# Performance work log

Measured on AMD Instinct MI355X. Metric: run time of the kernel, lower is better.

## Reference

```python
import jax, jax.numpy as jnp
import numpy as np

WS = 7
NH = 4

def _rel_idx(ws):
    ch, cw = np.meshgrid(np.arange(ws), np.arange(ws), indexing='ij')
    cf = np.stack([ch.ravel(), cw.ravel()])  # [2, ws*ws]
    rel = cf[:, :, None] - cf[:, None, :]
    rel = rel.transpose(1, 2, 0)
    rel[:, :, 0] += ws - 1
    rel[:, :, 1] += ws - 1
    rel[:, :, 0] *= 2 * ws - 1
    return jnp.asarray(rel.sum(-1), dtype=jnp.int32)  # [N, N]

def layernorm(x, g, b, eps=1e-5):
    m = jnp.mean(x, -1, keepdims=True)
    v = jnp.var(x, -1, keepdims=True)
    return (x - m) * jax.lax.rsqrt(v + eps) * g + b

def setup_inputs() -> dict:
    key = jax.random.key(0)
    ks = jax.random.split(key, 8)
    B, HH, WW, C = 32, 56, 56, 128
    hid = 512
    s = 0.02
    return {
        'x': jax.random.normal(ks[0], (B, HH * WW, C), jnp.float32),
        'H': HH, 'W': WW,
        'norm1_g': jnp.ones((C,), jnp.float32),
        'norm1_b': jnp.zeros((C,), jnp.float32),
        'qkv_w': jax.random.normal(ks[1], (3 * C, C), jnp.float32) * s,
        'qkv_b': jnp.zeros((3 * C,), jnp.float32),
        'rel_bias_table': jax.random.normal(ks[2], ((2 * WS - 1) ** 2, NH), jnp.float32) * s,
        'rel_idx': _rel_idx(WS),
        'proj_w': jax.random.normal(ks[3], (C, C), jnp.float32) * s,
        'proj_b': jnp.zeros((C,), jnp.float32),
        'norm2_g': jnp.ones((C,), jnp.float32),
        'norm2_b': jnp.zeros((C,), jnp.float32),
        'mlp_w1': jax.random.normal(ks[4], (hid, C), jnp.float32) * s,
        'mlp_b1': jnp.zeros((hid,), jnp.float32),
        'mlp_w2': jax.random.normal(ks[5], (C, hid), jnp.float32) * s,
        'mlp_b2': jnp.zeros((C,), jnp.float32),
    }

def swin_block(x, H, W, norm1_g, norm1_b, qkv_w, qkv_b, rel_bias_table, rel_idx,
               proj_w, proj_b, norm2_g, norm2_b, mlp_w1, mlp_b1, mlp_w2, mlp_b2,
               shift=3, ws=WS, nh=NH):
    B, L, C = x.shape
    N = ws * ws
    hd = C // nh
    scale = hd ** -0.5
    shortcut = x
    h = layernorm(x, norm1_g, norm1_b).reshape(B, H, W, C)
    if shift > 0:
        h = jnp.roll(h, (-shift, -shift), axis=(1, 2))
    # window partition -> [B*nW, N, C]
    h = h.reshape(B, H // ws, ws, W // ws, ws, C).transpose(0, 1, 3, 2, 4, 5).reshape(-1, N, C)
    # attention (no mask in source forward)
    qkv = h @ qkv_w.T + qkv_b  # [B_, N, 3C]
    qkv = qkv.reshape(-1, N, 3, nh, hd).transpose(2, 0, 3, 1, 4)
    q, k, v = qkv[0] * scale, qkv[1], qkv[2]  # [B_, nh, N, hd]
    attn = jnp.einsum('bhnd,bhmd->bhnm', q, k)
    bias = rel_bias_table[rel_idx.reshape(-1)].reshape(N, N, nh).transpose(2, 0, 1)
    attn = jax.nn.softmax(attn + bias[None], axis=-1)
    o = jnp.einsum('bhnm,bhmd->bhnd', attn, v).transpose(0, 2, 1, 3).reshape(-1, N, C)
    o = o @ proj_w.T + proj_b
    # window reverse -> [B, H, W, C]
    o = o.reshape(B, H // ws, W // ws, ws, ws, C).transpose(0, 1, 3, 2, 4, 5).reshape(B, H, W, C)
    if shift > 0:
        o = jnp.roll(o, (shift, shift), axis=(1, 2))
    x = shortcut + o.reshape(B, L, C)
    h2 = layernorm(x, norm2_g, norm2_b)
    h2 = jax.nn.gelu(h2 @ mlp_w1.T + mlp_b1, approximate=False) @ mlp_w2.T + mlp_b2
    return x + h2

def reference(x, H, W, norm1_g, norm1_b, qkv_w, qkv_b, rel_bias_table, rel_idx,
              proj_w, proj_b, norm2_g, norm2_b, mlp_w1, mlp_b1, mlp_w2, mlp_b2):
    return swin_block(x, H, W, norm1_g, norm1_b, qkv_w, qkv_b, rel_bias_table, rel_idx,
                      proj_w, proj_b, norm2_g, norm2_b, mlp_w1, mlp_b1, mlp_w2, mlp_b2)
```

## Files before the change

kernel.cpp:

```cpp
#include <hip/hip_runtime.h>
#include <hip/hip_bf16.h>


#define NWIN 2048

typedef short short8  __attribute__((ext_vector_type(8)));
typedef short short4v __attribute__((ext_vector_type(4)));
typedef float f32x4   __attribute__((ext_vector_type(4)));

#define QKVW_OFF  0
#define PROJW_OFF 49152
#define W1_OFF    65536
#define W2_OFF    131072
#define BIAS_BYTE_OFF 393216

__device__ __forceinline__ short f2bs(float v) {
  __hip_bfloat16 h = __float2bfloat16(v);
  union { __hip_bfloat16 h; short s; } u; u.h = h; return u.s;
}
__device__ __forceinline__ float gelu_f(float v) {
  float u = v * (0.7978845608028654f + 0.03567740814f * v * v);
  return v * __builtin_amdgcn_rcpf(1.f + __expf(-2.f * u));
}

__global__ __launch_bounds__(256) void conv_kernel(
    const float* __restrict__ qkvw, const float* __restrict__ projw,
    const float* __restrict__ w1,   const float* __restrict__ w2,
    const float* __restrict__ tab,  const int* __restrict__ ridx,
    __hip_bfloat16* __restrict__ wsb, float* __restrict__ biasT)
{
  int idx = blockIdx.x * 256 + threadIdx.x;
  if (idx < 49152)       wsb[QKVW_OFF + idx]          = __float2bfloat16(qkvw[idx]);
  else if (idx < 65536)  wsb[PROJW_OFF + idx - 49152] = __float2bfloat16(projw[idx - 49152]);
  else if (idx < 131072) wsb[W1_OFF + idx - 65536]    = __float2bfloat16(w1[idx - 65536]);
  else if (idx < 196608) wsb[W2_OFF + idx - 131072]   = __float2bfloat16(w2[idx - 131072]);
  else if (idx < 212992) {
    int i = idx - 196608;
    int h = i >> 12, m = (i >> 6) & 63, n = i & 63;
    biasT[i] = (m < 49 && n < 49) ? tab[ridx[n*49 + m]*4 + h] : 0.f;
  }
}

__global__ __launch_bounds__(512, 4) void fused_kernel(
    const float* __restrict__ x,
    const float* __restrict__ n1g, const float* __restrict__ n1b,
    const __hip_bfloat16* __restrict__ qkvwb, const float* __restrict__ qkvb,
    const float* __restrict__ biasT,
    const __hip_bfloat16* __restrict__ projwb, const float* __restrict__ projb,
    const float* __restrict__ n2g, const float* __restrict__ n2b,
    const __hip_bfloat16* __restrict__ w1b, const float* __restrict__ b1,
    const __hip_bfloat16* __restrict__ w2b, const float* __restrict__ b2,
    float* __restrict__ out)
{
  __shared__ alignas(16) __hip_bfloat16 hbuf[64][136];
  __shared__ alignas(16) char regA[40960];
  __shared__ alignas(16) __hip_bfloat16 vT[4][32][72];
  __hip_bfloat16* const qkb = (__hip_bfloat16*)regA;
  float*          const x2s = (float*)regA;
  __hip_bfloat16* const hb  = (__hip_bfloat16*)regA;

  const int tid = threadIdx.x, wave = tid >> 6, lane = tid & 63;
  const int l15 = lane & 15, quad = lane >> 4;
  const int b = blockIdx.x >> 6, wi = (blockIdx.x >> 3) & 7, wj = blockIdx.x & 7;

  {
    float g0 = n1g[lane], g1 = n1g[lane+64], e0 = n1b[lane], e1 = n1b[lane+64];
    float va[7], vb[7];
    #pragma unroll
    for (int i = 0; i < 7; ++i) {
      int n = wave + i*8;
      va[i] = 0.f; vb[i] = 0.f;
      if (n < 49) {
        int r = n / 7, c = n - r * 7;
        int si = wi*7 + r + 3; if (si >= 56) si -= 56;
        int sj = wj*7 + c + 3; if (sj >= 56) sj -= 56;
        const float* xr = x + (b*3136 + si*56 + sj) * 128;
        va[i] = xr[lane]; vb[i] = xr[lane + 64];
      }
    }
    #pragma unroll
    for (int i = 0; i < 7; ++i) {
      int n = wave + i*8;
      if (n < 49) {
        float s = va[i] + vb[i], sq = va[i]*va[i] + vb[i]*vb[i];
        #pragma unroll
        for (int off = 32; off > 0; off >>= 1) {
          s  += __shfl_xor(s,  off);
          sq += __shfl_xor(sq, off);
        }
        float mean = s * 0.0078125f;
        float var  = sq * 0.0078125f - mean*mean;
        float rstd = rsqrtf(var + 1e-5f);
        hbuf[n][lane]    = __float2bfloat16((va[i]-mean)*rstd*g0 + e0);
        hbuf[n][lane+64] = __float2bfloat16((vb[i]-mean)*rstd*g1 + e1);
      }
    }
  }
  __syncthreads();

  {
    const int t0 = wave * 3;
    f32x4 acc[3][4] = {};
    #pragma unroll
    for (int ks = 0; ks < 4; ++ks) {
      short8 hf[4];
      #pragma unroll
      for (int mt = 0; mt < 4; ++mt)
        hf[mt] = *(const short8*)(&hbuf[mt*16 + l15][ks*32 + quad*8]);
      #pragma unroll
      for (int ft = 0; ft < 3; ++ft) {
        short8 wf = *(const short8*)(qkvwb + ((t0 + ft)*16 + l15)*128 + ks*32 + quad*8);
        #pragma unroll
        for (int mt = 0; mt < 4; ++mt)
          acc[ft][mt] = __builtin_amdgcn_mfma_f32_16x16x32_bf16(wf, hf[mt], acc[ft][mt], 0, 0, 0);
      }
    }
    #pragma unroll
    for (int ft = 0; ft < 3; ++ft) {
      const int t = t0 + ft;
      if (t < 16) {
        const int which = t >> 3;
        const int fo = (t & 7) * 16 + quad * 4;
        const int hh = fo >> 5, d0 = fo & 31;
        const float qs = (t < 8) ? 0.17677669529663687f : 1.0f;
        float bb[4];
        #pragma unroll
        for (int r = 0; r < 4; ++r) bb[r] = qkvb[which*128 + fo + r];
        #pragma unroll
        for (int mt = 0; mt < 4; ++mt) {
          int m = mt*16 + l15;
          if (m < 49) {
            short4v pk;
            #pragma unroll
            for (int r = 0; r < 4; ++r) pk[r] = f2bs((acc[ft][mt][r] + bb[r]) * qs);
            *(short4v*)(qkb + ((hh*2 + which)*64 + m)*40 + d0) = pk;
          }
        }
      } else {
        const int nf = (t - 16) * 16 + quad * 4;
        const int hh = nf >> 5, d0 = nf & 31;
        float bb[4];
        #pragma unroll
        for (int r = 0; r < 4; ++r) bb[r] = qkvb[256 + nf + r];
        #pragma unroll
        for (int mt = 0; mt < 4; ++mt) {
          int m = mt*16 + l15;
          #pragma unroll
          for (int r = 0; r < 4; ++r) {
            float v = (m < 49) ? (acc[ft][mt][r] + bb[r]) : 0.f;
            vT[hh][d0 + r][m] = __float2bfloat16(v);
          }
        }
      }
    }
  }
  __syncthreads();

  {
    const int h = wave >> 1, half = wave & 1;
    __hip_bfloat16* qbase = qkb + (h*2 + 0)*64*40;
    __hip_bfloat16* kbase = qkb + (h*2 + 1)*64*40;
    short8 kf[4], qf[2];
    #pragma unroll
    for (int mt = 0; mt < 4; ++mt) kf[mt] = *(const short8*)(kbase + (mt*16 + l15)*40 + quad*8);
    #pragma unroll
    for (int nt = 0; nt < 2; ++nt)
      qf[nt] = *(const short8*)(qbase + ((half*2 + nt)*16 + l15)*40 + quad*8);
    const float* bT = biasT + h*4096;
    float bv[4][2][4];
    #pragma unroll
    for (int mt = 0; mt < 4; ++mt)
      #pragma unroll
      for (int nt = 0; nt < 2; ++nt)
        #pragma unroll
        for (int r = 0; r < 4; ++r)
          bv[mt][nt][r] = bT[(mt*16 + quad*4 + r)*64 + (half*2 + nt)*16 + l15];
    __syncthreads();

    f32x4 sacc[4][2] = {};
    #pragma unroll
    for (int mt = 0; mt < 4; ++mt)
      #pragma unroll
      for (int nt = 0; nt < 2; ++nt)
        sacc[mt][nt] = __builtin_amdgcn_mfma_f32_16x16x32_bf16(kf[mt], qf[nt], sacc[mt][nt], 0, 0, 0);

    #pragma unroll
    for (int mt = 0; mt < 4; ++mt)
      #pragma unroll
      for (int nt = 0; nt < 2; ++nt)
        #pragma unroll
        for (int r = 0; r < 4; ++r)
          sacc[mt][nt][r] += bv[mt][nt][r];

    __hip_bfloat16* pb = qbase;
    #pragma unroll
    for (int nt = 0; nt < 2; ++nt) {
      float mx = -1e30f;
      #pragma unroll
      for (int mt = 0; mt < 3; ++mt)
        #pragma unroll
        for (int r = 0; r < 4; ++r) mx = fmaxf(mx, sacc[mt][nt][r]);
      mx = fmaxf(mx, (quad == 0) ? sacc[3][nt][0] : -1e30f);
      mx = fmaxf(mx, __shfl_xor(mx, 16));
      mx = fmaxf(mx, __shfl_xor(mx, 32));
      float sum = 0.f;
      #pragma unroll
      for (int mt = 0; mt < 3; ++mt)
        #pragma unroll
        for (int r = 0; r < 4; ++r) {
          float e = __expf(sacc[mt][nt][r] - mx);
          sacc[mt][nt][r] = e; sum += e;
        }
      {
        float e = (quad == 0) ? __expf(sacc[3][nt][0] - mx) : 0.f;
        sacc[3][nt][0] = e; sacc[3][nt][1] = 0.f; sacc[3][nt][2] = 0.f; sacc[3][nt][3] = 0.f;
        sum += e;
      }
      sum += __shfl_xor(sum, 16);
      sum += __shfl_xor(sum, 32);
      float inv = 1.f / sum;
      int n = (half*2 + nt)*16 + l15;
      #pragma unroll
      for (int mt = 0; mt < 4; ++mt) {
        short4v pk;
        #pragma unroll
        for (int r = 0; r < 4; ++r) pk[r] = f2bs(sacc[mt][nt][r] * inv);
        *(short4v*)(pb + n*72 + mt*16 + quad*4) = pk;
      }
    }

    f32x4 oacc[2][2] = {};
    #pragma unroll
    for (int kt = 0; kt < 2; ++kt) {
      short8 vf[2], pf[2];
      #pragma unroll
      for (int dt = 0; dt < 2; ++dt)
        vf[dt] = *(const short8*)(&vT[h][dt*16 + l15][kt*32 + quad*8]);
      #pragma unroll
      for (int nc = 0; nc < 2; ++nc)
        pf[nc] = *(const short8*)(pb + ((half*2 + nc)*16 + l15)*72 + kt*32 + quad*8);
      #pragma unroll
      for (int dt = 0; dt < 2; ++dt)
        #pragma unroll
        for (int nc = 0; nc < 2; ++nc)
          oacc[dt][nc] = __builtin_amdgcn_mfma_f32_16x16x32_bf16(vf[dt], pf[nc], oacc[dt][nc], 0, 0, 0);
    }
    #pragma unroll
    for (int dt = 0; dt < 2; ++dt)
      #pragma unroll
      for (int nc = 0; nc < 2; ++nc) {
        int n = (half*2 + nc)*16 + l15;
        if (n < 49) {
          short4v pk;
          #pragma unroll
          for (int r = 0; r < 4; ++r) pk[r] = f2bs(oacc[dt][nc][r]);
          *(short4v*)(&hbuf[n][h*32 + dt*16 + quad*4]) = pk;
        }
      }
  }
  __syncthreads();

  f32x4 x2v[4];
  {
    const int ncol0 = wave * 16;
    const int n = ncol0 + l15;
    float xres[4][4];
    #pragma unroll
    for (int mt = 0; mt < 4; ++mt) {
      #pragma unroll
      for (int r = 0; r < 4; ++r) {
        int m = mt*16 + quad*4 + r;
        float v = 0.f;
        if (m < 49) {
          int rr = m / 7, cc = m - rr * 7;
          int si = wi*7 + rr + 3; if (si >= 56) si -= 56;
          int sj = wj*7 + cc + 3; if (sj >= 56) sj -= 56;
          v = x[(b*3136 + si*56 + sj) * 128 + n];
        }
        xres[mt][r] = v;
      }
    }
    f32x4 acc[4] = {};
    #pragma unroll
    for (int ks = 0; ks < 4; ++ks) {
      short8 af[4];
      #pragma unroll
      for (int mt = 0; mt < 4; ++mt)
        af[mt] = *(const short8*)(&hbuf[mt*16 + l15][ks*32 + quad*8]);
      short8 bfr = *(const short8*)(projwb + (ncol0 + l15)*128 + ks*32 + quad*8);
      #pragma unroll
      for (int mt = 0; mt < 4; ++mt)
        acc[mt] = __builtin_amdgcn_mfma_f32_16x16x32_bf16(af[mt], bfr, acc[mt], 0, 0, 0);
    }
    float pbv = projb[n];
    #pragma unroll
    for (int mt = 0; mt < 4; ++mt) {
      #pragma unroll
      for (int r = 0; r < 4; ++r) {
        int m = mt*16 + quad*4 + r;
        float v = 0.f;
        if (m < 49) v = acc[mt][r] + pbv + xres[mt][r];
        x2v[mt][r] = v;
        x2s[m*132 + n] = v;
      }
    }
  }
  __syncthreads();

  {
    float g0 = n2g[lane], g1 = n2g[lane+64], e0 = n2b[lane], e1 = n2b[lane+64];
    for (int n = wave; n < 49; n += 8) {
      float v0 = x2s[n*132 + lane], v1 = x2s[n*132 + lane + 64];
      float s = v0 + v1, sq = v0*v0 + v1*v1;
      #pragma unroll
      for (int off = 32; off > 0; off >>= 1) {
        s  += __shfl_xor(s,  off);
        sq += __shfl_xor(sq, off);
      }
      float mean = s * 0.0078125f;
      float var  = sq * 0.0078125f - mean*mean;
      float rstd = rsqrtf(var + 1e-5f);
      hbuf[n][lane]    = __float2bfloat16((v0-mean)*rstd*g0 + e0);
      hbuf[n][lane+64] = __float2bfloat16((v1-mean)*rstd*g1 + e1);
    }
    __hip_bfloat16 z = __float2bfloat16(0.f);
    for (int n = 49 + wave; n < 64; n += 8) {
      hbuf[n][lane] = z; hbuf[n][lane+64] = z;
    }
  }
  __syncthreads();

  f32x4 acc2[4] = {};
  #pragma unroll
  for (int chunk = 0; chunk < 2; ++chunk) {
    {
      const int jbl = wave * 32;
      f32x4 acc1[2][4] = {};
      #pragma unroll
      for (int ks = 0; ks < 4; ++ks) {
        short8 lf[4];
        #pragma unroll
        for (int mt = 0; mt < 4; ++mt)
          lf[mt] = *(const short8*)(&hbuf[mt*16 + l15][ks*32 + quad*8]);
        #pragma unroll
        for (int jt = 0; jt < 2; ++jt) {
          short8 wf = *(const short8*)(w1b + (chunk*256 + jbl + jt*16 + l15)*128 + ks*32 + quad*8);
          #pragma unroll
          for (int mt = 0; mt < 4; ++mt)
            acc1[jt][mt] = __builtin_amdgcn_mfma_f32_16x16x32_bf16(wf, lf[mt], acc1[jt][mt], 0, 0, 0);
        }
      }
      #pragma unroll
      for (int jt = 0; jt < 2; ++jt) {
        int j0l = jbl + jt*16 + quad*4;
        float bb[4];
        #pragma unroll
        for (int r = 0; r < 4; ++r) bb[r] = b1[chunk*256 + j0l + r];
        #pragma unroll
        for (int mt = 0; mt < 4; ++mt) {
          int m = mt*16 + l15;
          short4v pk;
          #pragma unroll
          for (int r = 0; r < 4; ++r) pk[r] = f2bs(gelu_f(acc1[jt][mt][r] + bb[r]));
          *(short4v*)(hb + m*264 + j0l) = pk;
        }
      }
    }
    __syncthreads();

    {
      const int fb2 = wave * 16;
      #pragma unroll
      for (int ks = 0; ks < 8; ++ks) {
        short8 af[4];
        #pragma unroll
        for (int mt = 0; mt < 4; ++mt)
          af[mt] = *(const short8*)(hb + (mt*16 + l15)*264 + ks*32 + quad*8);
        short8 bfr = *(const short8*)(w2b + (fb2 + l15)*512 + chunk*256 + ks*32 + quad*8);
        #pragma unroll
        for (int mt = 0; mt < 4; ++mt)
          acc2[mt] = __builtin_amdgcn_mfma_f32_16x16x32_bf16(af[mt], bfr, acc2[mt], 0, 0, 0);
      }
    }
    if (chunk == 0) __syncthreads();
  }

  {
    const int f = wave * 16 + l15;
    const float bb = b2[f];
    #pragma unroll
    for (int mt = 0; mt < 4; ++mt) {
      #pragma unroll
      for (int r = 0; r < 4; ++r) {
        int m = mt*16 + quad*4 + r;
        if (m < 49) {
          int rr = m / 7, cc = m - rr * 7;
          int si = wi*7 + rr + 3; if (si >= 56) si -= 56;
          int sj = wj*7 + cc + 3; if (sj >= 56) sj -= 56;
          int o = (b*3136 + si*56 + sj) * 128 + f;
          out[o] = acc2[mt][r] + bb + x2v[mt][r];
        }
      }
    }
  }
}

extern "C" void kernel_launch(void* const* d_in, const int* in_sizes, int n_in,
                              void* d_out, int out_size, void* d_ws, size_t ws_size,
                              hipStream_t stream) {
  const float* x     = (const float*)d_in[0];
  const float* n1g   = (const float*)d_in[3];
  const float* n1b   = (const float*)d_in[4];
  const float* qkvw  = (const float*)d_in[5];
  const float* qkvb  = (const float*)d_in[6];
  const float* tab   = (const float*)d_in[7];
  const int*   ridx  = (const int*)d_in[8];
  const float* projw = (const float*)d_in[9];
  const float* projb = (const float*)d_in[10];
  const float* n2g   = (const float*)d_in[11];
  const float* n2b   = (const float*)d_in[12];
  const float* w1    = (const float*)d_in[13];
  const float* b1    = (const float*)d_in[14];
  const float* w2    = (const float*)d_in[15];
  const float* b2    = (const float*)d_in[16];
  float* outp = (float*)d_out;

  __hip_bfloat16* wsb = (__hip_bfloat16*)d_ws;
  float* biasT = (float*)((char*)d_ws + BIAS_BYTE_OFF);

  hipLaunchKernelGGL(conv_kernel, dim3(832), dim3(256), 0, stream,
                     qkvw, projw, w1, w2, tab, ridx, wsb, biasT);
  hipLaunchKernelGGL(fused_kernel, dim3(NWIN), dim3(512), 0, stream,
                     x, n1g, n1b, wsb + QKVW_OFF, qkvb, biasT, wsb + PROJW_OFF, projb,
                     n2g, n2b, wsb + W1_OFF, b1, wsb + W2_OFF, b2, outp);
}
```

Before: 262.1 us.

## Prefetch weight fragments into registers ahead of barriers across GEMM stages

The fused Swin block kernel now issues global loads of weight fragments into registers earlier: QKV weights at kernel start, the proj weights and residual x during the attention stage, and W1 chunk 0 and W2 fragments before the preceding barriers. The MLP chunk loop is manually unrolled so that each W2 slice is loaded before its sync. The aim is to hide global and L2 load latency behind LDS work and barriers instead of stalling in front of the MFMAs. In exchange, register pressure rises considerably (dozens of extra short8 values live at once), which could lower occupancy or cause spills.

```diff
diff --git a/kernel.cpp b/kernel.cpp
--- a/kernel.cpp
+++ b/kernel.cpp
@@ -63,6 +63,16 @@
   const int l15 = lane & 15, quad = lane >> 4;
   const int b = blockIdx.x >> 6, wi = (blockIdx.x >> 3) & 7, wj = blockIdx.x & 7;
 
+  short8 wreg[3][4];
+  {
+    const int t0 = wave * 3;
+    #pragma unroll
+    for (int ft = 0; ft < 3; ++ft)
+      #pragma unroll
+      for (int ks = 0; ks < 4; ++ks)
+        wreg[ft][ks] = *(const short8*)(qkvwb + ((t0 + ft)*16 + l15)*128 + ks*32 + quad*8);
+  }
+
   {
     float g0 = n1g[lane], g1 = n1g[lane+64], e0 = n1b[lane], e1 = n1b[lane+64];
     float va[7], vb[7];
@@ -109,10 +119,9 @@
         hf[mt] = *(const short8*)(&hbuf[mt*16 + l15][ks*32 + quad*8]);
       #pragma unroll
       for (int ft = 0; ft < 3; ++ft) {
-        short8 wf = *(const short8*)(qkvwb + ((t0 + ft)*16 + l15)*128 + ks*32 + quad*8);
         #pragma unroll
         for (int mt = 0; mt < 4; ++mt)
-          acc[ft][mt] = __builtin_amdgcn_mfma_f32_16x16x32_bf16(wf, hf[mt], acc[ft][mt], 0, 0, 0);
+          acc[ft][mt] = __builtin_amdgcn_mfma_f32_16x16x32_bf16(wreg[ft][ks], hf[mt], acc[ft][mt], 0, 0, 0);
       }
     }
     #pragma unroll
@@ -156,6 +165,8 @@
   }
   __syncthreads();
 
+  short8 pw[4];
+  float xres[4][4];
   {
     const int h = wave >> 1, half = wave & 1;
     __hip_bfloat16* qbase = qkb + (h*2 + 0)*64*40;
@@ -257,14 +268,11 @@
           *(short4v*)(&hbuf[n][h*32 + dt*16 + quad*4]) = pk;
         }
       }
-  }
-  __syncthreads();
-
-  f32x4 x2v[4];
-  {
-    const int ncol0 = wave * 16;
-    const int n = ncol0 + l15;
-    float xres[4][4];
+
+    const int ncol0 = wave * 16, n4 = ncol0 + l15;
+    #pragma unroll
+    for (int ks = 0; ks < 4; ++ks)
+      pw[ks] = *(const short8*)(projwb + n4*128 + ks*32 + quad*8);
     #pragma unroll
     for (int mt = 0; mt < 4; ++mt) {
       #pragma unroll
@@ -275,11 +283,17 @@
           int rr = m / 7, cc = m - rr * 7;
           int si = wi*7 + rr + 3; if (si >= 56) si -= 56;
           int sj = wj*7 + cc + 3; if (sj >= 56) sj -= 56;
-          v = x[(b*3136 + si*56 + sj) * 128 + n];
+          v = x[(b*3136 + si*56 + sj) * 128 + n4];
         }
         xres[mt][r] = v;
       }
     }
+  }
+  __syncthreads();
+
+  f32x4 x2v[4];
+  {
+    const int n = wave * 16 + l15;
     f32x4 acc[4] = {};
     #pragma unroll
     for (int ks = 0; ks < 4; ++ks) {
@@ -287,10 +301,9 @@
       #pragma unroll
       for (int mt = 0; mt < 4; ++mt)
         af[mt] = *(const short8*)(&hbuf[mt*16 + l15][ks*32 + quad*8]);
-      short8 bfr = *(const short8*)(projwb + (ncol0 + l15)*128 + ks*32 + quad*8);
       #pragma unroll
       for (int mt = 0; mt < 4; ++mt)
-        acc[mt] = __builtin_amdgcn_mfma_f32_16x16x32_bf16(af[mt], bfr, acc[mt], 0, 0, 0);
+        acc[mt] = __builtin_amdgcn_mfma_f32_16x16x32_bf16(af[mt], pw[ks], acc[mt], 0, 0, 0);
     }
     float pbv = projb[n];
     #pragma unroll
@@ -328,65 +341,121 @@
       hbuf[n][lane] = z; hbuf[n][lane+64] = z;
     }
   }
+
+  short8 w1f0[4][2];
+  {
+    const int jbl = wave * 32;
+    #pragma unroll
+    for (int ks = 0; ks < 4; ++ks)
+      #pragma unroll
+      for (int jt = 0; jt < 2; ++jt)
+        w1f0[ks][jt] = *(const short8*)(w1b + (jbl + jt*16 + l15)*128 + ks*32 + quad*8);
+  }
   __syncthreads();
 
   f32x4 acc2[4] = {};
+  short8 w2f[8];
+  const int fb2 = wave * 16;
+
+  {
+    const int jbl = wave * 32;
+    f32x4 acc1[2][4] = {};
+    #pragma unroll
+    for (int ks = 0; ks < 4; ++ks) {
+      short8 lf[4];
+      #pragma unroll
+      for (int mt = 0; mt < 4; ++mt)
+        lf[mt] = *(const short8*)(&hbuf[mt*16 + l15][ks*32 + quad*8]);
+      #pragma unroll
+      for (int jt = 0; jt < 2; ++jt)
+        #pragma unroll
+        for (int mt = 0; mt < 4; ++mt)
+          acc1[jt][mt] = __builtin_amdgcn_mfma_f32_16x16x32_bf16(w1f0[ks][jt], lf[mt], acc1[jt][mt], 0, 0, 0);
+    }
+    #pragma unroll
+    for (int jt = 0; jt < 2; ++jt) {
+      int j0l = jbl + jt*16 + quad*4;
+      float bb[4];
+      #pragma unroll
+      for (int r = 0; r < 4; ++r) bb[r] = b1[j0l + r];
+      #pragma unroll
+      for (int mt = 0; mt < 4; ++mt) {
+        int m = mt*16 + l15;
+        short4v pk;
+        #pragma unroll
+        for (int r = 0; r < 4; ++r) pk[r] = f2bs(gelu_f(acc1[jt][mt][r] + bb[r]));
+        *(short4v*)(hb + m*264 + j0l) = pk;
+      }
+    }
+  }
   #pragma unroll
-  for (int chunk = 0; chunk < 2; ++chunk) {
-    {
-      const int jbl = wave * 32;
-      f32x4 acc1[2][4] = {};
-      #pragma unroll
-      for (int ks = 0; ks < 4; ++ks) {
-        short8 lf[4];
+  for (int ks = 0; ks < 8; ++ks)
+    w2f[ks] = *(const short8*)(w2b + (fb2 + l15)*512 + ks*32 + quad*8);
+  __syncthreads();
+
+  #pragma unroll
+  for (int ks = 0; ks < 8; ++ks) {
+    short8 af[4];
+    #pragma unroll
+    for (int mt = 0; mt < 4; ++mt)
+      af[mt] = *(const short8*)(hb + (mt*16 + l15)*264 + ks*32 + quad*8);
+    #pragma unroll
+    for (int mt = 0; mt < 4; ++mt)
+      acc2[mt] = __builtin_amdgcn_mfma_f32_16x16x32_bf16(af[mt], w2f[ks], acc2[mt], 0, 0, 0);
+  }
+  __syncthreads();
+
+  {
+    const int jbl = wave * 32;
+    f32x4 acc1[2][4] = {};
+    #pragma unroll
+    for (int ks = 0; ks < 4; ++ks) {
+      short8 lf[4];
+      #pragma unroll
+      for (int mt = 0; mt < 4; ++mt)
+        lf[mt] = *(const short8*)(&hbuf[mt*16 + l15][ks*32 + quad*8]);
+      #pragma unroll
+      for (int jt = 0; jt < 2; ++jt) {
+        short8 wf = *(const short8*)(w1b + (256 + jbl + jt*16 + l15)*128 + ks*32 + quad*8);
         #pragma unroll
         for (int mt = 0; mt < 4; ++mt)
-          lf[mt] = *(const short8*)(&hbuf[mt*16 + l15][ks*32 + quad*8]);
-        #pragma unroll
-        for (int jt = 0; jt < 2; ++jt) {
-          short8 wf = *(const short8*)(w1b + (chunk*256 + jbl + jt*16 + l15)*128 + ks*32 + quad*8);
-          #pragma unroll
-          for (int mt = 0; mt < 4; ++mt)
-            acc1[jt][mt] = __builtin_amdgcn_mfma_f32_16x16x32_bf16(wf, lf[mt], acc1[jt][mt], 0, 0, 0);
-        }
-      }
-      #pragma unroll
-      for (int jt = 0; jt < 2; ++jt) {
-        int j0l = jbl + jt*16 + quad*4;
-        float bb[4];
-        #pragma unroll
-        for (int r = 0; r < 4; ++r) bb[r] = b1[chunk*256 + j0l + r];
-        #pragma unroll
-        for (int mt = 0; mt < 4; ++mt) {
-          int m = mt*16 + l15;
-          short4v pk;
-          #pragma unroll
-          for (int r = 0; r < 4; ++r) pk[r] = f2bs(gelu_f(acc1[jt][mt][r] + bb[r]));
-          *(short4v*)(hb + m*264 + j0l) = pk;
-        }
-      }
-    }
-    __syncthreads();
-
-    {
-      const int fb2 = wave * 16;
-      #pragma unroll
-      for (int ks = 0; ks < 8; ++ks) {
-        short8 af[4];
-        #pragma unroll
-        for (int mt = 0; mt < 4; ++mt)
-          af[mt] = *(const short8*)(hb + (mt*16 + l15)*264 + ks*32 + quad*8);
-        short8 bfr = *(const short8*)(w2b + (fb2 + l15)*512 + chunk*256 + ks*32 + quad*8);
-        #pragma unroll
-        for (int mt = 0; mt < 4; ++mt)
-          acc2[mt] = __builtin_amdgcn_mfma_f32_16x16x32_bf16(af[mt], bfr, acc2[mt], 0, 0, 0);
-      }
-    }
-    if (chunk == 0) __syncthreads();
-  }
-
-  {
-    const int f = wave * 16 + l15;
+          acc1[jt][mt] = __builtin_amdgcn_mfma_f32_16x16x32_bf16(wf, lf[mt], acc1[jt][mt], 0, 0, 0);
+      }
+    }
+    #pragma unroll
+    for (int jt = 0; jt < 2; ++jt) {
+      int j0l = jbl + jt*16 + quad*4;
+      float bb[4];
+      #pragma unroll
+      for (int r = 0; r < 4; ++r) bb[r] = b1[256 + j0l + r];
+      #pragma unroll
+      for (int mt = 0; mt < 4; ++mt) {
+        int m = mt*16 + l15;
+        short4v pk;
+        #pragma unroll
+        for (int r = 0; r < 4; ++r) pk[r] = f2bs(gelu_f(acc1[jt][mt][r] + bb[r]));
+        *(short4v*)(hb + m*264 + j0l) = pk;
+      }
+    }
+  }
+  #pragma unroll
+  for (int ks = 0; ks < 8; ++ks)
+    w2f[ks] = *(const short8*)(w2b + (fb2 + l15)*512 + 256 + ks*32 + quad*8);
+  __syncthreads();
+
+  #pragma unroll
+  for (int ks = 0; ks < 8; ++ks) {
+    short8 af[4];
+    #pragma unroll
+    for (int mt = 0; mt < 4; ++mt)
+      af[mt] = *(const short8*)(hb + (mt*16 + l15)*264 + ks*32 + quad*8);
+    #pragma unroll
+    for (int mt = 0; mt < 4; ++mt)
+      acc2[mt] = __builtin_amdgcn_mfma_f32_16x16x32_bf16(af[mt], w2f[ks], acc2[mt], 0, 0, 0);
+  }
+
+  {
+    const int f = fb2 + l15;
     const float bb = b2[f];
     #pragma unroll
     for (int mt = 0; mt < 4; ++mt) {
```

New measurement: 256.7 us, median of 2. 1.02x faster.

## Cut LDS footprint: keep Q/P in registers, swizzle V, double-buffer MLP chunks

Applied to the files above, without the earlier changes.

Q is now computed per wave directly in registers and the softmax probabilities are repacked into MFMA fragments with lane shuffles, so neither round-trips through shared memory. V is stored transposed with an XOR swizzle to avoid bank conflicts. The MLP hidden layer is split into four 128-wide chunks over two ping-pong LDS buffers, which lets GEMM1 of one chunk overlap GEMM2 of the previous one. Total LDS shrinks and launch bounds rise from 4 to 6 blocks per CU to raise occupancy, at the risk of register pressure and extra shuffle work.

```diff
diff --git a/kernel.cpp b/kernel.cpp
--- a/kernel.cpp
+++ b/kernel.cpp
@@ -7,6 +7,8 @@
 typedef short short8  __attribute__((ext_vector_type(8)));
 typedef short short4v __attribute__((ext_vector_type(4)));
 typedef float f32x4   __attribute__((ext_vector_type(4)));
+
+union Frag { int i[4]; unsigned u[4]; short8 s; };
 
 #define QKVW_OFF  0
 #define PROJW_OFF 49152
@@ -41,7 +43,7 @@
   }
 }
 
-__global__ __launch_bounds__(512, 4) void fused_kernel(
+__global__ __launch_bounds__(512, 6) void fused_kernel(
     const float* __restrict__ x,
     const float* __restrict__ n1g, const float* __restrict__ n1b,
     const __hip_bfloat16* __restrict__ qkvwb, const float* __restrict__ qkvb,
@@ -53,14 +55,16 @@
     float* __restrict__ out)
 {
   __shared__ alignas(16) __hip_bfloat16 hbuf[64][136];
-  __shared__ alignas(16) char regA[40960];
-  __shared__ alignas(16) __hip_bfloat16 vT[4][32][72];
-  __hip_bfloat16* const qkb = (__hip_bfloat16*)regA;
-  float*          const x2s = (float*)regA;
-  __hip_bfloat16* const hb  = (__hip_bfloat16*)regA;
+  __shared__ alignas(16) char shmem[36864];
+  __hip_bfloat16* const Kl  = (__hip_bfloat16*)shmem;
+  __hip_bfloat16* const vTl = (__hip_bfloat16*)(shmem + 20480);
+  float*          const x2s = (float*)shmem;
+  __hip_bfloat16* const hbA = (__hip_bfloat16*)shmem;
+  __hip_bfloat16* const hbB = (__hip_bfloat16*)(shmem + 17408);
 
   const int tid = threadIdx.x, wave = tid >> 6, lane = tid & 63;
   const int l15 = lane & 15, quad = lane >> 4;
+  const int h = wave >> 1, half = wave & 1;
   const int b = blockIdx.x >> 6, wi = (blockIdx.x >> 3) & 7, wj = blockIdx.x & 7;
 
   {
@@ -99,108 +103,131 @@
   __syncthreads();
 
   {
-    const int t0 = wave * 3;
-    f32x4 acc[3][4] = {};
+    f32x4 kacc[4] = {}, vacc[4] = {};
     #pragma unroll
     for (int ks = 0; ks < 4; ++ks) {
       short8 hf[4];
       #pragma unroll
       for (int mt = 0; mt < 4; ++mt)
         hf[mt] = *(const short8*)(&hbuf[mt*16 + l15][ks*32 + quad*8]);
-      #pragma unroll
-      for (int ft = 0; ft < 3; ++ft) {
-        short8 wf = *(const short8*)(qkvwb + ((t0 + ft)*16 + l15)*128 + ks*32 + quad*8);
-        #pragma unroll
-        for (int mt = 0; mt < 4; ++mt)
-          acc[ft][mt] = __builtin_amdgcn_mfma_f32_16x16x32_bf16(wf, hf[mt], acc[ft][mt], 0, 0, 0);
-      }
-    }
-    #pragma unroll
-    for (int ft = 0; ft < 3; ++ft) {
-      const int t = t0 + ft;
-      if (t < 16) {
-        const int which = t >> 3;
-        const int fo = (t & 7) * 16 + quad * 4;
-        const int hh = fo >> 5, d0 = fo & 31;
-        const float qs = (t < 8) ? 0.17677669529663687f : 1.0f;
-        float bb[4];
-        #pragma unroll
-        for (int r = 0; r < 4; ++r) bb[r] = qkvb[which*128 + fo + r];
-        #pragma unroll
-        for (int mt = 0; mt < 4; ++mt) {
-          int m = mt*16 + l15;
-          if (m < 49) {
-            short4v pk;
-            #pragma unroll
-            for (int r = 0; r < 4; ++r) pk[r] = f2bs((acc[ft][mt][r] + bb[r]) * qs);
-            *(short4v*)(qkb + ((hh*2 + which)*64 + m)*40 + d0) = pk;
-          }
-        }
-      } else {
-        const int nf = (t - 16) * 16 + quad * 4;
-        const int hh = nf >> 5, d0 = nf & 31;
-        float bb[4];
-        #pragma unroll
-        for (int r = 0; r < 4; ++r) bb[r] = qkvb[256 + nf + r];
-        #pragma unroll
-        for (int mt = 0; mt < 4; ++mt) {
-          int m = mt*16 + l15;
+      short8 wfk = *(const short8*)(qkvwb + (128 + wave*16 + l15)*128 + ks*32 + quad*8);
+      short8 wfv = *(const short8*)(qkvwb + (256 + wave*16 + l15)*128 + ks*32 + quad*8);
+      #pragma unroll
+      for (int mt = 0; mt < 4; ++mt) {
+        kacc[mt] = __builtin_amdgcn_mfma_f32_16x16x32_bf16(wfk, hf[mt], kacc[mt], 0, 0, 0);
+        vacc[mt] = __builtin_amdgcn_mfma_f32_16x16x32_bf16(hf[mt], wfv, vacc[mt], 0, 0, 0);
+      }
+    }
+    {
+      const int fo = wave*16 + quad*4;
+      const int hh = wave >> 1, d0 = fo & 31;
+      float bb[4];
+      #pragma unroll
+      for (int r = 0; r < 4; ++r) bb[r] = qkvb[128 + fo + r];
+      #pragma unroll
+      for (int mt = 0; mt < 4; ++mt) {
+        int m = mt*16 + l15;
+        if (m < 49) {
+          short4v pkv;
           #pragma unroll
-          for (int r = 0; r < 4; ++r) {
-            float v = (m < 49) ? (acc[ft][mt][r] + bb[r]) : 0.f;
-            vT[hh][d0 + r][m] = __float2bfloat16(v);
-          }
-        }
-      }
-    }
-  }
-  __syncthreads();
-
-  {
-    const int h = wave >> 1, half = wave & 1;
-    __hip_bfloat16* qbase = qkb + (h*2 + 0)*64*40;
-    __hip_bfloat16* kbase = qkb + (h*2 + 1)*64*40;
-    short8 kf[4], qf[2];
-    #pragma unroll
-    for (int mt = 0; mt < 4; ++mt) kf[mt] = *(const short8*)(kbase + (mt*16 + l15)*40 + quad*8);
+          for (int r = 0; r < 4; ++r) pkv[r] = f2bs(kacc[mt][r] + bb[r]);
+          *(short4v*)(Kl + (hh*64 + m)*40 + d0) = pkv;
+        }
+      }
+    }
+    {
+      const int fv = wave*16 + l15;
+      const int hh = wave >> 1, d = fv & 31;
+      const float bia = qkvb[256 + fv];
+      #pragma unroll
+      for (int mt = 0; mt < 4; ++mt) {
+        int m0 = mt*16 + quad*4;
+        #pragma unroll
+        for (int r = 0; r < 4; ++r) {
+          int m = m0 + r;
+          float v = (m < 49) ? (vacc[mt][r] + bia) : 0.f;
+          vTl[(hh*32 + d)*64 + ((((m>>3) ^ (d & 7))) << 3) + (m & 7)] = __float2bfloat16(v);
+        }
+      }
+    }
+  }
+
+  Frag qfr[2];
+  {
+    f32x4 qacc[2][2] = {};
+    #pragma unroll
+    for (int ks = 0; ks < 4; ++ks) {
+      short8 hfq[2];
+      #pragma unroll
+      for (int nt = 0; nt < 2; ++nt)
+        hfq[nt] = *(const short8*)(&hbuf[(half*2 + nt)*16 + l15][ks*32 + quad*8]);
+      #pragma unroll
+      for (int tq = 0; tq < 2; ++tq) {
+        short8 wf = *(const short8*)(qkvwb + ((h*2 + tq)*16 + l15)*128 + ks*32 + quad*8);
+        #pragma unroll
+        for (int nt = 0; nt < 2; ++nt)
+          qacc[tq][nt] = __builtin_amdgcn_mfma_f32_16x16x32_bf16(wf, hfq[nt], qacc[tq][nt], 0, 0, 0);
+      }
+    }
+    const float qs = 0.17677669529663687f;
+    unsigned pkq[2][2][2];
+    #pragma unroll
+    for (int tq = 0; tq < 2; ++tq) {
+      float bb[4];
+      #pragma unroll
+      for (int r = 0; r < 4; ++r) bb[r] = qkvb[h*32 + tq*16 + quad*4 + r];
+      #pragma unroll
+      for (int nt = 0; nt < 2; ++nt)
+        #pragma unroll
+        for (int i = 0; i < 2; ++i) {
+          unsigned lo = (unsigned short)f2bs((qacc[tq][nt][2*i]   + bb[2*i])   * qs);
+          unsigned hi = (unsigned short)f2bs((qacc[tq][nt][2*i+1] + bb[2*i+1]) * qs);
+          pkq[tq][nt][i] = lo | (hi << 16);
+        }
+    }
     #pragma unroll
     for (int nt = 0; nt < 2; ++nt)
-      qf[nt] = *(const short8*)(qbase + ((half*2 + nt)*16 + l15)*40 + quad*8);
+      #pragma unroll
+      for (int p = 0; p < 4; ++p) {
+        int sl = (((quad & 1)*2 + (p >> 1)) << 4) | l15;
+        int a  = __shfl((int)pkq[0][nt][p & 1], sl);
+        int c2 = __shfl((int)pkq[1][nt][p & 1], sl);
+        qfr[nt].i[p] = (quad >= 2) ? c2 : a;
+      }
+  }
+  __syncthreads();
+
+  {
+    short8 kf[4];
+    #pragma unroll
+    for (int mt = 0; mt < 4; ++mt)
+      kf[mt] = *(const short8*)(Kl + (h*64 + mt*16 + l15)*40 + quad*8);
+
+    f32x4 sacc[4][2] = {};
+    #pragma unroll
+    for (int mt = 0; mt < 4; ++mt)
+      #pragma unroll
+      for (int nc = 0; nc < 2; ++nc)
+        sacc[mt][nc] = __builtin_amdgcn_mfma_f32_16x16x32_bf16(kf[mt], qfr[nc].s, sacc[mt][nc], 0, 0, 0);
+
     const float* bT = biasT + h*4096;
-    float bv[4][2][4];
     #pragma unroll
     for (int mt = 0; mt < 4; ++mt)
       #pragma unroll
-      for (int nt = 0; nt < 2; ++nt)
+      for (int nc = 0; nc < 2; ++nc)
         #pragma unroll
         for (int r = 0; r < 4; ++r)
-          bv[mt][nt][r] = bT[(mt*16 + quad*4 + r)*64 + (half*2 + nt)*16 + l15];
-    __syncthreads();
-
-    f32x4 sacc[4][2] = {};
-    #pragma unroll
-    for (int mt = 0; mt < 4; ++mt)
-      #pragma unroll
-      for (int nt = 0; nt < 2; ++nt)
-        sacc[mt][nt] = __builtin_amdgcn_mfma_f32_16x16x32_bf16(kf[mt], qf[nt], sacc[mt][nt], 0, 0, 0);
-
-    #pragma unroll
-    for (int mt = 0; mt < 4; ++mt)
-      #pragma unroll
-      for (int nt = 0; nt < 2; ++nt)
-        #pragma unroll
-        for (int r = 0; r < 4; ++r)
-          sacc[mt][nt][r] += bv[mt][nt][r];
-
-    __hip_bfloat16* pb = qbase;
-    #pragma unroll
-    for (int nt = 0; nt < 2; ++nt) {
+          sacc[mt][nc][r] += bT[(mt*16 + quad*4 + r)*64 + (half*2 + nc)*16 + l15];
+
+    unsigned pk[4][2][2];
+    #pragma unroll
+    for (int nc = 0; nc < 2; ++nc) {
       float mx = -1e30f;
       #pragma unroll
       for (int mt = 0; mt < 3; ++mt)
         #pragma unroll
-        for (int r = 0; r < 4; ++r) mx = fmaxf(mx, sacc[mt][nt][r]);
-      mx = fmaxf(mx, (quad == 0) ? sacc[3][nt][0] : -1e30f);
+        for (int r = 0; r < 4; ++r) mx = fmaxf(mx, sacc[mt][nc][r]);
+      mx = fmaxf(mx, (quad == 0) ? sacc[3][nc][0] : -1e30f);
       mx = fmaxf(mx, __shfl_xor(mx, 16));
       mx = fmaxf(mx, __shfl_xor(mx, 32));
       float sum = 0.f;
@@ -208,42 +235,51 @@
       for (int mt = 0; mt < 3; ++mt)
         #pragma unroll
         for (int r = 0; r < 4; ++r) {
-          float e = __expf(sacc[mt][nt][r] - mx);
-          sacc[mt][nt][r] = e; sum += e;
+          float e = __expf(sacc[mt][nc][r] - mx);
+          sacc[mt][nc][r] = e; sum += e;
         }
       {
-        float e = (quad == 0) ? __expf(sacc[3][nt][0] - mx) : 0.f;
-        sacc[3][nt][0] = e; sacc[3][nt][1] = 0.f; sacc[3][nt][2] = 0.f; sacc[3][nt][3] = 0.f;
+        float e = (quad == 0) ? __expf(sacc[3][nc][0] - mx) : 0.f;
+        sacc[3][nc][0] = e; sacc[3][nc][1] = 0.f; sacc[3][nc][2] = 0.f; sacc[3][nc][3] = 0.f;
         sum += e;
       }
       sum += __shfl_xor(sum, 16);
       sum += __shfl_xor(sum, 32);
       float inv = 1.f / sum;
-      int n = (half*2 + nt)*16 + l15;
-      #pragma unroll
-      for (int mt = 0; mt < 4; ++mt) {
-        short4v pk;
-        #pragma unroll
-        for (int r = 0; r < 4; ++r) pk[r] = f2bs(sacc[mt][nt][r] * inv);
-        *(short4v*)(pb + n*72 + mt*16 + quad*4) = pk;
-      }
-    }
+      #pragma unroll
+      for (int mt = 0; mt < 4; ++mt)
+        #pragma unroll
+        for (int i = 0; i < 2; ++i) {
+          unsigned lo = (unsigned short)f2bs(sacc[mt][nc][2*i]   * inv);
+          unsigned hi = (unsigned short)f2bs(sacc[mt][nc][2*i+1] * inv);
+          pk[mt][nc][i] = lo | (hi << 16);
+        }
+    }
+    Frag pfr[2][2];
+    #pragma unroll
+    for (int kt = 0; kt < 2; ++kt)
+      #pragma unroll
+      for (int nc = 0; nc < 2; ++nc)
+        #pragma unroll
+        for (int p = 0; p < 4; ++p) {
+          int sl = (((quad & 1)*2 + (p >> 1)) << 4) | l15;
+          int a  = __shfl((int)pk[kt*2    ][nc][p & 1], sl);
+          int c2 = __shfl((int)pk[kt*2 + 1][nc][p & 1], sl);
+          pfr[kt][nc].i[p] = (quad >= 2) ? c2 : a;
+        }
 
     f32x4 oacc[2][2] = {};
     #pragma unroll
     for (int kt = 0; kt < 2; ++kt) {
-      short8 vf[2], pf[2];
+      short8 vf[2];
       #pragma unroll
       for (int dt = 0; dt < 2; ++dt)
-        vf[dt] = *(const short8*)(&vT[h][dt*16 + l15][kt*32 + quad*8]);
-      #pragma unroll
-      for (int nc = 0; nc < 2; ++nc)
-        pf[nc] = *(const short8*)(pb + ((half*2 + nc)*16 + l15)*72 + kt*32 + quad*8);
+        vf[dt] = *(const short8*)(vTl + (h*32 + dt*16 + l15)*64 + (((kt*4 + quad) ^ (l15 & 7)) << 3));
       #pragma unroll
       for (int dt = 0; dt < 2; ++dt)
         #pragma unroll
         for (int nc = 0; nc < 2; ++nc)
-          oacc[dt][nc] = __builtin_amdgcn_mfma_f32_16x16x32_bf16(vf[dt], pf[nc], oacc[dt][nc], 0, 0, 0);
+          oacc[dt][nc] = __builtin_amdgcn_mfma_f32_16x16x32_bf16(vf[dt], pfr[kt][nc].s, oacc[dt][nc], 0, 0, 0);
     }
     #pragma unroll
     for (int dt = 0; dt < 2; ++dt)
@@ -251,10 +287,10 @@
       for (int nc = 0; nc < 2; ++nc) {
         int n = (half*2 + nc)*16 + l15;
         if (n < 49) {
-          short4v pk;
+          short4v pkv;
           #pragma unroll
-          for (int r = 0; r < 4; ++r) pk[r] = f2bs(oacc[dt][nc][r]);
-          *(short4v*)(&hbuf[n][h*32 + dt*16 + quad*4]) = pk;
+          for (int r = 0; r < 4; ++r) pkv[r] = f2bs(oacc[dt][nc][r]);
+          *(short4v*)(&hbuf[n][h*32 + dt*16 + quad*4]) = pkv;
         }
       }
   }
@@ -262,8 +298,7 @@
 
   f32x4 x2v[4];
   {
-    const int ncol0 = wave * 16;
-    const int n = ncol0 + l15;
+    const int n = wave * 16 + l15;
     float xres[4][4];
     #pragma unroll
     for (int mt = 0; mt < 4; ++mt) {
@@ -287,7 +322,7 @@
       #pragma unroll
       for (int mt = 0; mt < 4; ++mt)
         af[mt] = *(const short8*)(&hbuf[mt*16 + l15][ks*32 + quad*8]);
-      short8 bfr = *(const short8*)(projwb + (ncol0 + l15)*128 + ks*32 + quad*8);
+      short8 bfr = *(const short8*)(projwb + n*128 + ks*32 + quad*8);
       #pragma unroll
       for (int mt = 0; mt < 4; ++mt)
         acc[mt] = __builtin_amdgcn_mfma_f32_16x16x32_bf16(af[mt], bfr, acc[mt], 0, 0, 0);
@@ -331,62 +366,60 @@
   __syncthreads();
 
   f32x4 acc2[4] = {};
-  #pragma unroll
-  for (int chunk = 0; chunk < 2; ++chunk) {
-    {
-      const int jbl = wave * 32;
-      f32x4 acc1[2][4] = {};
-      #pragma unroll
-      for (int ks = 0; ks < 4; ++ks) {
-        short8 lf[4];
-        #pragma unroll
-        for (int mt = 0; mt < 4; ++mt)
-          lf[mt] = *(const short8*)(&hbuf[mt*16 + l15][ks*32 + quad*8]);
-        #pragma unroll
-        for (int jt = 0; jt < 2; ++jt) {
-          short8 wf = *(const short8*)(w1b + (chunk*256 + jbl + jt*16 + l15)*128 + ks*32 + quad*8);
-          #pragma unroll
-          for (int mt = 0; mt < 4; ++mt)
-            acc1[jt][mt] = __builtin_amdgcn_mfma_f32_16x16x32_bf16(wf, lf[mt], acc1[jt][mt], 0, 0, 0);
-        }
-      }
-      #pragma unroll
-      for (int jt = 0; jt < 2; ++jt) {
-        int j0l = jbl + jt*16 + quad*4;
-        float bb[4];
-        #pragma unroll
-        for (int r = 0; r < 4; ++r) bb[r] = b1[chunk*256 + j0l + r];
-        #pragma unroll
-        for (int mt = 0; mt < 4; ++mt) {
-          int m = mt*16 + l15;
-          short4v pk;
-          #pragma unroll
-          for (int r = 0; r < 4; ++r) pk[r] = f2bs(gelu_f(acc1[jt][mt][r] + bb[r]));
-          *(short4v*)(hb + m*264 + j0l) = pk;
-        }
-      }
-    }
-    __syncthreads();
-
-    {
-      const int fb2 = wave * 16;
-      #pragma unroll
-      for (int ks = 0; ks < 8; ++ks) {
-        short8 af[4];
-        #pragma unroll
-        for (int mt = 0; mt < 4; ++mt)
-          af[mt] = *(const short8*)(hb + (mt*16 + l15)*264 + ks*32 + quad*8);
-        short8 bfr = *(const short8*)(w2b + (fb2 + l15)*512 + chunk*256 + ks*32 + quad*8);
-        #pragma unroll
-        for (int mt = 0; mt < 4; ++mt)
-          acc2[mt] = __builtin_amdgcn_mfma_f32_16x16x32_bf16(af[mt], bfr, acc2[mt], 0, 0, 0);
-      }
-    }
-    if (chunk == 0) __syncthreads();
-  }
-
-  {
-    const int f = wave * 16 + l15;
+  const int fb2 = wave * 16;
+
+  auto G1 = [&](int c, __hip_bfloat16* dst) {
+    const int jg = c*128 + wave*16;
+    f32x4 a1[4] = {};
+    #pragma unroll
+    for (int ks = 0; ks < 4; ++ks) {
+      short8 lf[4];
+      #pragma unroll
+      for (int mt = 0; mt < 4; ++mt)
+        lf[mt] = *(const short8*)(&hbuf[mt*16 + l15][ks*32 + quad*8]);
+      short8 wf = *(const short8*)(w1b + (jg + l15)*128 + ks*32 + quad*8);
+      #pragma unroll
+      for (int mt = 0; mt < 4; ++mt)
+        a1[mt] = __builtin_amdgcn_mfma_f32_16x16x32_bf16(wf, lf[mt], a1[mt], 0, 0, 0);
+    }
+    float bb[4];
+    #pragma unroll
+    for (int r = 0; r < 4; ++r) bb[r] = b1[jg + quad*4 + r];
+    #pragma unroll
+    for (int mt = 0; mt < 4; ++mt) {
+      int m = mt*16 + l15;
+      short4v pkv;
+      #pragma unroll
+      for (int r = 0; r < 4; ++r) pkv[r] = f2bs(gelu_f(a1[mt][r] + bb[r]));
+      *(short4v*)(dst + m*136 + wave*16 + quad*4) = pkv;
+    }
+  };
+  auto G2 = [&](int c, const __hip_bfloat16* src) {
+    #pragma unroll
+    for (int ks = 0; ks < 4; ++ks) {
+      short8 af[4];
+      #pragma unroll
+      for (int mt = 0; mt < 4; ++mt)
+        af[mt] = *(const short8*)(src + (mt*16 + l15)*136 + ks*32 + quad*8);
+      short8 wf = *(const short8*)(w2b + (fb2 + l15)*512 + c*128 + ks*32 + quad*8);
+      #pragma unroll
+      for (int mt = 0; mt < 4; ++mt)
+        acc2[mt] = __builtin_amdgcn_mfma_f32_16x16x32_bf16(af[mt], wf, acc2[mt], 0, 0, 0);
+    }
+  };
+
+  G1(0, hbA);
+  __syncthreads();
+  G1(1, hbB); G2(0, hbA);
+  __syncthreads();
+  G1(2, hbA); G2(1, hbB);
+  __syncthreads();
+  G1(3, hbB); G2(2, hbA);
+  __syncthreads();
+  G2(3, hbB);
+
+  {
+    const int f = fb2 + l15;
     const float bb = b2[f];
     #pragma unroll
     for (int mt = 0; mt < 4; ++mt) {
```

Result: slower. 304.9 us (+16.3%).
